# Optimization experiments

Hardware: AMD Instinct MI355X
Metric: run time of the kernel (lower is better)

The kernel has to match this reference:

```python
import jax, jax.numpy as jnp
import numpy as np

EPS = 1e-5        # torch LayerNorm default eps
INNER = 4
AFFECT_W = 0.3
BATCH = 65536
DIM = 128


def _ln(x, g, b):
    m = jnp.mean(x, axis=-1, keepdims=True)
    v = jnp.var(x, axis=-1, keepdims=True)
    return (x - m) * jax.lax.rsqrt(v + EPS) * g + b


def _gelu(x):
    return jax.nn.gelu(x, approximate=False)  # torch nn.GELU default (erf)


def setup_inputs() -> dict:
    key = jax.random.key(0)
    ks = jax.random.split(key, 18)
    B, d = BATCH, DIM

    def W(k, i, o):
        return jax.random.normal(k, (i, o), jnp.float32) / np.float32(np.sqrt(i))

    return {
        "x": jax.random.normal(ks[0], (B, d), jnp.float32),
        "y_init": jax.random.normal(ks[1], (B, d), jnp.float32),
        "affect_vec": jax.random.normal(ks[2], (B, 3), jnp.float32),
        "ln_latent_g": jnp.ones((3 * d,), jnp.float32), "ln_latent_b": jnp.zeros((3 * d,), jnp.float32),
        "ln_answer_g": jnp.ones((2 * d,), jnp.float32), "ln_answer_b": jnp.zeros((2 * d,), jnp.float32),
        "ln_z_g": jnp.ones((d,), jnp.float32), "ln_z_b": jnp.zeros((d,), jnp.float32),
        "lat_w1": W(ks[3], 3 * d, 2 * d), "lat_b1": jnp.zeros((2 * d,), jnp.float32),
        "lat_w2": W(ks[4], 2 * d, d), "lat_b2": jnp.zeros((d,), jnp.float32),
        "ans_w1": W(ks[5], 2 * d, 2 * d), "ans_b1": jnp.zeros((2 * d,), jnp.float32),
        "ans_w2": W(ks[6], 2 * d, d), "ans_b2": jnp.zeros((d,), jnp.float32),
        "aff_w": W(ks[7], 3, d), "aff_b": jnp.zeros((d,), jnp.float32),
        "gate_w": W(ks[8], 2 * d, 1), "gate_b": jnp.zeros((1,), jnp.float32),
        "q_w": W(ks[9], d, d), "q_b": jnp.zeros((d,), jnp.float32),
        "k_w": W(ks[10], d, d), "k_b": jnp.zeros((d,), jnp.float32),
        "v_w": W(ks[11], d, d), "v_b": jnp.zeros((d,), jnp.float32),
        "o_w": W(ks[12], d, d), "o_b": jnp.zeros((d,), jnp.float32),
        "pad_w1": W(ks[13], d, d // 2), "pad_b1": jnp.zeros((d // 2,), jnp.float32),
        "pad_w2": W(ks[14], d // 2, 3), "pad_b2": jnp.zeros((3,), jnp.float32),
        "K": 5,
    }


def _forward(x, y_init, affect_vec, ln_latent_g, ln_latent_b, ln_answer_g, ln_answer_b,
             ln_z_g, ln_z_b, lat_w1, lat_b1, lat_w2, lat_b2, ans_w1, ans_b1, ans_w2, ans_b2,
             aff_w, aff_b, gate_w, gate_b, q_w, q_b, k_w, k_b, v_w, v_b, o_w, o_b,
             pad_w1, pad_b1, pad_w2, pad_b2, K):
    d = x.shape[-1]
    scale = jnp.float32(d) ** -0.5
    y = y_init
    z = jnp.zeros_like(y)
    confs = []     # scalar gate means (detached, like .item() in torch)
    history = []   # list of [B, 1, d] z snapshots
    memory = []    # SoulKernel memory buffer: list of [d] rinse_state[0] snapshots
    for _ in range(K):
        for _ in range(INNER):
            li = _ln(jnp.concatenate([x, y, z], axis=-1), ln_latent_g, ln_latent_b)
            z_delta = _gelu(li @ lat_w1 + lat_b1) @ lat_w2 + lat_b2
            z = _ln(z + 0.3 * z_delta, ln_z_g, ln_z_b)
        affect_latent = jnp.tanh(affect_vec @ aff_w + aff_b)          # [B, d]
        gate = jax.nn.sigmoid(jnp.concatenate([z, affect_latent], axis=-1) @ gate_w + gate_b)  # [B, 1]
        z = z + AFFECT_W * gate * affect_latent
        confs.append(jax.lax.stop_gradient(jnp.mean(gate)))
        history.append(z[:, None, :])
        if len(history) > 1:
            seq = jnp.concatenate(history, axis=1)  # [B, t, d]
            Q = seq @ q_w + q_b
            Kt = seq @ k_w + k_b
            V = seq @ v_w + v_b
            attn = jax.nn.softmax(jnp.einsum('bsd,btd->bst', Q, Kt) * scale, axis=-1)
            attn_out = jnp.einsum('bst,btd->bsd', attn, V) @ o_w + o_b
            z = _ln(z + attn_out[:, -1, :], ln_z_g, ln_z_b)
        rinse = jnp.tanh(z + y)
        # SoulKernel (hope is computed but unused in the original)
        faith = jnp.sqrt(sum(confs) / len(confs))
        z = z + faith * 0.05 * z
        future = jnp.mean(jnp.stack(memory[-3:]), axis=0) if memory else jnp.zeros((d,), x.dtype)  # [d]
        bond = jnp.tanh(jax.lax.stop_gradient(jnp.mean(x * z)) + jax.lax.stop_gradient(jnp.mean(y * rinse)))
        z = z + 0.2 * bond * (future - z)
        rinse = jnp.tanh(rinse + future * 0.3)
        memory.append(jax.lax.stop_gradient(rinse[0]))
        ai = _ln(jnp.concatenate([y, z], axis=-1), ln_answer_g, ln_answer_b)
        y = y + 0.4 * (_gelu(ai @ ans_w1 + ans_b1) @ ans_w2 + ans_b2)
    pad = jnp.tanh(_gelu(z @ pad_w1 + pad_b1) @ pad_w2 + pad_b2)
    return y, jnp.stack(confs), pad


def reference(x, y_init, affect_vec, ln_latent_g, ln_latent_b, ln_answer_g, ln_answer_b,
              ln_z_g, ln_z_b, lat_w1, lat_b1, lat_w2, lat_b2, ans_w1, ans_b1, ans_w2, ans_b2,
              aff_w, aff_b, gate_w, gate_b, q_w, q_b, k_w, k_b, v_w, v_b, o_w, o_b,
              pad_w1, pad_b1, pad_w2, pad_b2, K):
    return _forward(x, y_init, affect_vec, ln_latent_g, ln_latent_b, ln_answer_g, ln_answer_b,
                    ln_z_g, ln_z_b, lat_w1, lat_b1, lat_w2, lat_b2, ans_w1, ans_b1, ans_w2, ans_b2,
                    aff_w, aff_b, gate_w, gate_b, q_w, q_b, k_w, k_b, v_w, v_b, o_w, o_b,
                    pad_w1, pad_b1, pad_w2, pad_b2, K)
```

## Files before the change

kernel.cpp:

```cpp
#include <hip/hip_runtime.h>
#include <math.h>


#define BATCH 65536
#define D 128
#define BD ((size_t)BATCH * D)
#define NSTEP 5
#define ROWS 32
#define NTHR 256
#define NBLK (BATCH / ROWS)
#define LN_EPS 1e-5f
#define ATT_SCALE 0.08838834764831845f
#define LDA 132
#define LDB 260

#define WS_Z    ((size_t)0)
#define WS_H1   (BD)
#define WS_PART (WS_H1 + 5*BD)
#define WS_SCAL (WS_PART + (size_t)NBLK*4)
#define WS_H2   (WS_SCAL + 2048)
#define WS_KV_END (WS_H2 + 5*BD)

#define SC_FS   0
#define SC_B02  1
#define SC_CSUM 2
#define SC_FUT  16
#define SC_MEM  256
#define SC_R10  960

struct Args {
  const float *x, *y_init, *affect;
  const float *g_lat, *b_lat, *g_ans, *b_ans, *g_z, *b_z;
  const float *lw1, *lb1, *lw2, *lb2;
  const float *aw1, *ab1, *aw2, *ab2;
  const float *affw, *affb, *gw, *gb;
  const float *qw, *qb, *kw, *kb, *vw, *vb, *ow, *ob;
  const float *pw1, *pb1, *pw2, *pb2;
  float *Y, *conf, *pad;
  float *Z, *H1, *H2, *PART, *SCAL;
  int useKV;
};

__device__ __forceinline__ float4 ld4(const float* p) { return *(const float4*)p; }
__device__ __forceinline__ void st4(float* p, float4 v) { *(float4*)p = v; }
__device__ __forceinline__ float geluf(float v) { return 0.5f*v*(1.0f + erff(v*0.70710678118654752f)); }
__device__ __forceinline__ float dot4(float4 a, float4 b){ return a.x*b.x + a.y*b.y + a.z*b.z + a.w*b.w; }
__device__ __forceinline__ void accSQ(float4 v, float& S, float& Q) {
  S += v.x+v.y+v.z+v.w;
  Q += v.x*v.x + v.y*v.y + v.z*v.z + v.w*v.w;
}

template<int KDIM, int NPT>
__device__ __forceinline__ void mm_block(const float* __restrict__ W, int N,
                                         const float* As, int lda,
                                         int rg, int cg, float (&acc)[4][NPT])
{
  const float* a0 = As + (rg*4+0)*lda;
  const float* a1 = As + (rg*4+1)*lda;
  const float* a2 = As + (rg*4+2)*lda;
  const float* a3 = As + (rg*4+3)*lda;
  const float* wp = W + cg*NPT;
  #pragma unroll 4
  for (int k = 0; k < KDIM; ++k) {
    float w[NPT];
    if constexpr (NPT == 8) {
      float4 w0 = ld4(wp + (size_t)k*N);
      float4 w1 = ld4(wp + (size_t)k*N + 4);
      w[0]=w0.x; w[1]=w0.y; w[2]=w0.z; w[3]=w0.w;
      w[4]=w1.x; w[5]=w1.y; w[6]=w1.z; w[7]=w1.w;
    } else if constexpr (NPT == 4) {
      float4 w0 = ld4(wp + (size_t)k*N);
      w[0]=w0.x; w[1]=w0.y; w[2]=w0.z; w[3]=w0.w;
    } else {
      float2 w0 = *(const float2*)(wp + (size_t)k*N);
      w[0]=w0.x; w[1]=w0.y;
    }
    float av0=a0[k], av1=a1[k], av2=a2[k], av3=a3[k];
    #pragma unroll
    for (int c = 0; c < NPT; ++c) {
      acc[0][c] += av0*w[c];
      acc[1][c] += av1*w[c];
      acc[2][c] += av2*w[c];
      acc[3][c] += av3*w[c];
    }
  }
}

__device__ __forceinline__ void z_ln_update(const Args& A, int row0, int rg, int cg,
                                            const float (&add)[4][4])
{
  float4 g4 = ld4(A.g_z + cg*4);
  float4 b4 = ld4(A.b_z + cg*4);
  #pragma unroll
  for (int rr = 0; rr < 4; ++rr) {
    size_t off = (size_t)(row0 + rg*4 + rr)*D + cg*4;
    float4 z = ld4(A.Z + off);
    float v0 = z.x + add[rr][0];
    float v1 = z.y + add[rr][1];
    float v2 = z.z + add[rr][2];
    float v3 = z.w + add[rr][3];
    float S = v0+v1+v2+v3;
    float Q = v0*v0+v1*v1+v2*v2+v3*v3;
    S += __shfl_xor(S,1);  Q += __shfl_xor(Q,1);
    S += __shfl_xor(S,2);  Q += __shfl_xor(Q,2);
    S += __shfl_xor(S,4);  Q += __shfl_xor(Q,4);
    S += __shfl_xor(S,8);  Q += __shfl_xor(Q,8);
    S += __shfl_xor(S,16); Q += __shfl_xor(Q,16);
    float m  = S*(1.f/128.f);
    float rs = rsqrtf(Q*(1.f/128.f) - m*m + LN_EPS);
    float4 o;
    o.x = (v0-m)*rs*g4.x + b4.x;
    o.y = (v1-m)*rs*g4.y + b4.y;
    o.z = (v2-m)*rs*g4.z + b4.z;
    o.w = (v3-m)*rs*g4.w + b4.w;
    st4(A.Z + off, o);
  }
}

__device__ __forceinline__ void stage_raw(float* sA, const float* src, int row0, int t)
{
  for (int e4 = t; e4 < ROWS*32; e4 += NTHR) {
    int r = e4 >> 5, c4 = e4 & 31;
    st4(sA + r*LDA + c4*4, ld4(src + (size_t)(row0+r)*D + c4*4));
  }
}

__device__ __forceinline__ void epilogue_phase(const Args& A, float* sB, float* sM, float* sR,
                                               int row0, int t, int rg, int cg, int r8, int sub)
{
  const float fs  = A.SCAL[SC_FS];
  const float b02 = A.SCAL[SC_B02];
  const float a   = fs*(1.0f - b02);
  for (int e4 = t; e4 < ROWS*32; e4 += NTHR) {
    int r = e4 >> 5, c4 = e4 & 31;
    size_t off = (size_t)(row0 + r)*D + c4*4;
    float4 z = ld4(A.Z + off);
    float4 f = ld4(A.SCAL + SC_FUT + c4*4);
    z.x = z.x*a + b02*f.x;
    z.y = z.y*a + b02*f.y;
    z.z = z.z*a + b02*f.z;
    z.w = z.w*a + b02*f.w;
    st4(A.Z + off, z);
  }
  __syncthreads();
  {
    const float* yr = A.Y + (size_t)(row0 + r8)*D;
    const float* zr = A.Z + (size_t)(row0 + r8)*D;
    float S = 0.f, Q = 0.f;
    #pragma unroll
    for (int j = 0; j < 4; ++j) {
      int c = (sub + 8*j)*4;
      accSQ(ld4(yr + c), S, Q);
      accSQ(ld4(zr + c), S, Q);
    }
    S += __shfl_xor(S,1); Q += __shfl_xor(Q,1);
    S += __shfl_xor(S,2); Q += __shfl_xor(Q,2);
    S += __shfl_xor(S,4); Q += __shfl_xor(Q,4);
    if (sub == 0) {
      float m = S*(1.f/256.f);
      sM[r8] = m;
      sR[r8] = rsqrtf(Q*(1.f/256.f) - m*m + LN_EPS);
    }
  }
  __syncthreads();
  for (int e4 = t; e4 < ROWS*64; e4 += NTHR) {
    int r = e4 >> 6, c4 = e4 & 63;
    int k = c4*4;
    float m = sM[r], rs = sR[r];
    float4 v = (k < D) ? ld4(A.Y + (size_t)(row0+r)*D + k)
                       : ld4(A.Z + (size_t)(row0+r)*D + (k - D));
    float4 g = ld4(A.g_ans + k);
    float4 b = ld4(A.b_ans + k);
    float4 o;
    o.x = (v.x-m)*rs*g.x + b.x;
    o.y = (v.y-m)*rs*g.y + b.y;
    o.z = (v.z-m)*rs*g.z + b.z;
    o.w = (v.w-m)*rs*g.w + b.w;
    st4(sB + r*LDB + k, o);
  }
  __syncthreads();
  float acc[4][8] = {};
  mm_block<256,8>(A.aw1, 256, sB, LDB, rg, cg, acc);
  float4 b1a = ld4(A.ab1 + cg*8);
  float4 b1b = ld4(A.ab1 + cg*8 + 4);
  float h[4][8];
  #pragma unroll
  for (int rr = 0; rr < 4; ++rr) {
    h[rr][0]=geluf(acc[rr][0]+b1a.x); h[rr][1]=geluf(acc[rr][1]+b1a.y);
    h[rr][2]=geluf(acc[rr][2]+b1a.z); h[rr][3]=geluf(acc[rr][3]+b1a.w);
    h[rr][4]=geluf(acc[rr][4]+b1b.x); h[rr][5]=geluf(acc[rr][5]+b1b.y);
    h[rr][6]=geluf(acc[rr][6]+b1b.z); h[rr][7]=geluf(acc[rr][7]+b1b.w);
  }
  __syncthreads();
  #pragma unroll
  for (int rr = 0; rr < 4; ++rr) {
    float4 h0; h0.x=h[rr][0]; h0.y=h[rr][1]; h0.z=h[rr][2]; h0.w=h[rr][3];
    float4 h1; h1.x=h[rr][4]; h1.y=h[rr][5]; h1.z=h[rr][6]; h1.w=h[rr][7];
    st4(sB + (rg*4+rr)*LDB + cg*8,     h0);
    st4(sB + (rg*4+rr)*LDB + cg*8 + 4, h1);
  }
  __syncthreads();
  float acc2[4][4] = {};
  mm_block<256,4>(A.aw2, 128, sB, LDB, rg, cg, acc2);
  float4 b2 = ld4(A.ab2 + cg*4);
  #pragma unroll
  for (int rr = 0; rr < 4; ++rr) {
    size_t off = (size_t)(row0 + rg*4 + rr)*D + cg*4;
    float4 y = ld4(A.Y + off);
    y.x += 0.4f*(acc2[rr][0] + b2.x);
    y.y += 0.4f*(acc2[rr][1] + b2.y);
    y.z += 0.4f*(acc2[rr][2] + b2.z);
    y.w += 0.4f*(acc2[rr][3] + b2.w);
    st4(A.Y + off, y);
  }
  __syncthreads();
}

__global__ void prepK(Args A)
{
  size_t i  = (size_t)blockIdx.x*blockDim.x + threadIdx.x;
  size_t n4 = BD/4;
  float4 zero; zero.x=0.f; zero.y=0.f; zero.z=0.f; zero.w=0.f;
  for (; i < n4; i += (size_t)gridDim.x*blockDim.x) {
    ((float4*)A.Z)[i] = zero;
    ((float4*)A.Y)[i] = ((const float4*)A.y_init)[i];
  }
}

template<int STEP>
__global__ __launch_bounds__(NTHR, 2) void stepK(Args A)
{
  __shared__ __align__(16) float sA[ROWS*LDA];
  __shared__ __align__(16) float sB[ROWS*LDB];
  __shared__ float sM[ROWS], sR[ROWS], sG[ROWS];
  __shared__ float sS[ROWS][8];
  __shared__ float sRed[4][2];

  const int t = threadIdx.x;
  const int row0 = blockIdx.x * ROWS;
  const int rg = t >> 5, cg = t & 31;
  const int r8 = t >> 3, sub = t & 7;

  if (STEP > 0)
    epilogue_phase(A, sB, sM, sR, row0, t, rg, cg, r8, sub);

  #pragma unroll 1
  for (int it = 0; it < 4; ++it) {
    {
      const float* xr = A.x + (size_t)(row0 + r8)*D;
      const float* yr = A.Y + (size_t)(row0 + r8)*D;
      const float* zr = A.Z + (size_t)(row0 + r8)*D;
      float S = 0.f, Q = 0.f;
      #pragma unroll
      for (int j = 0; j < 4; ++j) {
        int c = (sub + 8*j)*4;
        accSQ(ld4(xr + c), S, Q);
        accSQ(ld4(yr + c), S, Q);
        accSQ(ld4(zr + c), S, Q);
      }
      S += __shfl_xor(S,1); Q += __shfl_xor(Q,1);
      S += __shfl_xor(S,2); Q += __shfl_xor(Q,2);
      S += __shfl_xor(S,4); Q += __shfl_xor(Q,4);
      if (sub == 0) {
        float m = S*(1.f/384.f);
        sM[r8] = m;
        sR[r8] = rsqrtf(Q*(1.f/384.f) - m*m + LN_EPS);
      }
    }
    __syncthreads();
    float acc[4][8] = {};
    #pragma unroll 1
    for (int seg = 0; seg < 3; ++seg) {
      const float* src = (seg == 0) ? A.x : (seg == 1 ? (const float*)A.Y : (const float*)A.Z);
      for (int e4 = t; e4 < ROWS*32; e4 += NTHR) {
        int r = e4 >> 5, c4 = e4 & 31;
        float4 v = ld4(src + (size_t)(row0+r)*D + c4*4);
        float m = sM[r], rs = sR[r];
        int k = seg*D + c4*4;
        float4 g = ld4(A.g_lat + k);
        float4 b = ld4(A.b_lat + k);
        float4 o;
        o.x = (v.x-m)*rs*g.x + b.x;
        o.y = (v.y-m)*rs*g.y + b.y;
        o.z = (v.z-m)*rs*g.z + b.z;
        o.w = (v.w-m)*rs*g.w + b.w;
        st4(sA + r*LDA + c4*4, o);
      }
      __syncthreads();
      mm_block<128,8>(A.lw1 + (size_t)seg*D*256, 256, sA, LDA, rg, cg, acc);
      __syncthreads();
    }
    float4 l1a = ld4(A.lb1 + cg*8);
    float4 l1b = ld4(A.lb1 + cg*8 + 4);
    #pragma unroll
    for (int rr = 0; rr < 4; ++rr) {
      float4 h0, h1;
      h0.x = geluf(acc[rr][0]+l1a.x); h0.y = geluf(acc[rr][1]+l1a.y);
      h0.z = geluf(acc[rr][2]+l1a.z); h0.w = geluf(acc[rr][3]+l1a.w);
      h1.x = geluf(acc[rr][4]+l1b.x); h1.y = geluf(acc[rr][5]+l1b.y);
      h1.z = geluf(acc[rr][6]+l1b.z); h1.w = geluf(acc[rr][7]+l1b.w);
      st4(sB + (rg*4+rr)*LDB + cg*8,     h0);
      st4(sB + (rg*4+rr)*LDB + cg*8 + 4, h1);
    }
    __syncthreads();
    float acc2[4][4] = {};
    mm_block<256,4>(A.lw2, 128, sB, LDB, rg, cg, acc2);
    float4 l2 = ld4(A.lb2 + cg*4);
    float add[4][4];
    #pragma unroll
    for (int rr = 0; rr < 4; ++rr) {
      add[rr][0] = 0.3f*(acc2[rr][0]+l2.x);
      add[rr][1] = 0.3f*(acc2[rr][1]+l2.y);
      add[rr][2] = 0.3f*(acc2[rr][2]+l2.z);
      add[rr][3] = 0.3f*(acc2[rr][3]+l2.w);
    }
    z_ln_update(A, row0, rg, cg, add);
    __syncthreads();
  }

  {
    size_t row = (size_t)row0 + r8;
    const float* zr = A.Z + row*D;
    float af0 = A.affect[row*3+0];
    float af1 = A.affect[row*3+1];
    float af2 = A.affect[row*3+2];
    float dg = 0.f;
    #pragma unroll
    for (int j = 0; j < 4; ++j) {
      int c = (sub + 8*j)*4;
      float4 zv = ld4(zr + c);
      float4 g1 = ld4(A.gw + c);
      float4 g2 = ld4(A.gw + D + c);
      float4 w0 = ld4(A.affw + c);
      float4 w1 = ld4(A.affw + D + c);
      float4 w2 = ld4(A.affw + 2*D + c);
      float4 ab = ld4(A.affb + c);
      float4 al;
      al.x = tanhf(af0*w0.x + af1*w1.x + af2*w2.x + ab.x);
      al.y = tanhf(af0*w0.y + af1*w1.y + af2*w2.y + ab.y);
      al.z = tanhf(af0*w0.z + af1*w1.z + af2*w2.z + ab.z);
      al.w = tanhf(af0*w0.w + af1*w1.w + af2*w2.w + ab.w);
      st4(sA + r8*LDA + c, al);
      dg += dot4(zv, g1) + dot4(al, g2);
    }
    dg += __shfl_xor(dg,1);
    dg += __shfl_xor(dg,2);
    dg += __shfl_xor(dg,4);
    if (sub == 0) sG[r8] = 1.f/(1.f + expf(-(dg + A.gb[0])));
  }
  __syncthreads();
  {
    float* zhw = A.H1 + (size_t)STEP*BD;
    for (int e4 = t; e4 < ROWS*32; e4 += NTHR) {
      int r = e4 >> 5, c4 = e4 & 31;
      size_t off = (size_t)(row0+r)*D + c4*4;
      float4 z  = ld4(A.Z + off);
      float4 al = ld4(sA + r*LDA + c4*4);
      float g = 0.3f * sG[r];
      z.x += g*al.x; z.y += g*al.y; z.z += g*al.z; z.w += g*al.w;
      st4(A.Z + off, z);
      if (!A.useKV) st4(zhw + off, z);
    }
  }
  __syncthreads();

  float q[4][4];
  if (A.useKV || STEP > 0) {
    stage_raw(sA, A.Z, row0, t);
    __syncthreads();
  }
  if (A.useKV) {
    float kacc[4][4] = {}, vacc[4][4] = {};
    mm_block<128,4>(A.kw, 128, sA, LDA, rg, cg, kacc);
    mm_block<128,4>(A.vw, 128, sA, LDA, rg, cg, vacc);
    float4 kb4 = ld4(A.kb + cg*4);
    float4 vb4 = ld4(A.vb + cg*4);
    float* KH = A.H1 + (size_t)STEP*BD;
    float* VH = A.H2 + (size_t)STEP*BD;
    #pragma unroll
    for (int rr = 0; rr < 4; ++rr) {
      size_t off = (size_t)(row0 + rg*4 + rr)*D + cg*4;
      float4 kv; kv.x=kacc[rr][0]+kb4.x; kv.y=kacc[rr][1]+kb4.y;
                 kv.z=kacc[rr][2]+kb4.z; kv.w=kacc[rr][3]+kb4.w;
      float4 vv; vv.x=vacc[rr][0]+vb4.x; vv.y=vacc[rr][1]+vb4.y;
                 vv.z=vacc[rr][2]+vb4.z; vv.w=vacc[rr][3]+vb4.w;
      st4(KH + off, kv);
      st4(VH + off, vv);
    }
  }
  if (STEP > 0) {
    float qacc[4][4] = {};
    mm_block<128,4>(A.qw, 128, sA, LDA, rg, cg, qacc);
    float4 qb4 = ld4(A.qb + cg*4);
    #pragma unroll
    for (int rr = 0; rr < 4; ++rr) {
      q[rr][0]=qacc[rr][0]+qb4.x; q[rr][1]=qacc[rr][1]+qb4.y;
      q[rr][2]=qacc[rr][2]+qb4.z; q[rr][3]=qacc[rr][3]+qb4.w;
    }
  }

  if (STEP > 0) {
    if (A.useKV) {
      #pragma unroll 1
      for (int j = 0; j <= STEP; ++j) {
        const float* KH = A.H1 + (size_t)j*BD;
        #pragma unroll
        for (int rr = 0; rr < 4; ++rr) {
          float4 kv = ld4(KH + (size_t)(row0 + rg*4 + rr)*D + cg*4);
          float s = q[rr][0]*kv.x + q[rr][1]*kv.y + q[rr][2]*kv.z + q[rr][3]*kv.w;
          s += __shfl_xor(s,1); s += __shfl_xor(s,2); s += __shfl_xor(s,4);
          s += __shfl_xor(s,8); s += __shfl_xor(s,16);
          if (cg == 0) sS[rg*4+rr][j] = s;
        }
      }
    } else {
      #pragma unroll 1
      for (int j = 0; j <= STEP; ++j) {
        __syncthreads();
        stage_raw(sA, A.H1 + (size_t)j*BD, row0, t);
        __syncthreads();
        float kacc[4][4] = {};
        mm_block<128,4>(A.kw, 128, sA, LDA, rg, cg, kacc);
        float4 kb4 = ld4(A.kb + cg*4);
        #pragma unroll
        for (int rr = 0; rr < 4; ++rr) {
          float s = q[rr][0]*(kacc[rr][0]+kb4.x) + q[rr][1]*(kacc[rr][1]+kb4.y)
                  + q[rr][2]*(kacc[rr][2]+kb4.z) + q[rr][3]*(kacc[rr][3]+kb4.w);
          s += __shfl_xor(s,1); s += __shfl_xor(s,2); s += __shfl_xor(s,4);
          s += __shfl_xor(s,8); s += __shfl_xor(s,16);
          if (cg == 0) sS[rg*4+rr][j] = s;
        }
      }
    }
    __syncthreads();
    if (t < ROWS) {
      float mx = -3.0e38f;
      for (int j = 0; j <= STEP; ++j) { float v = sS[t][j]*ATT_SCALE; sS[t][j] = v; mx = fmaxf(mx, v); }
      float sum = 0.f;
      for (int j = 0; j <= STEP; ++j) { float p = expf(sS[t][j]-mx); sS[t][j] = p; sum += p; }
      float inv = 1.f/sum;
      for (int j = 0; j <= STEP; ++j) sS[t][j] *= inv;
    }
    __syncthreads();
    float ao[4][4] = {};
    if (A.useKV) {
      #pragma unroll 1
      for (int j = 0; j <= STEP; ++j) {
        const float* VH = A.H2 + (size_t)j*BD;
        #pragma unroll
        for (int rr = 0; rr < 4; ++rr) {
          float p = sS[rg*4+rr][j];
          float4 vv = ld4(VH + (size_t)(row0 + rg*4 + rr)*D + cg*4);
          ao[rr][0] += p*vv.x; ao[rr][1] += p*vv.y;
          ao[rr][2] += p*vv.z; ao[rr][3] += p*vv.w;
        }
      }
    } else {
      #pragma unroll 1
      for (int j = 0; j <= STEP; ++j) {
        __syncthreads();
        stage_raw(sA, A.H1 + (size_t)j*BD, row0, t);
        __syncthreads();
        float vacc[4][4] = {};
        mm_block<128,4>(A.vw, 128, sA, LDA, rg, cg, vacc);
        float4 vb4 = ld4(A.vb + cg*4);
        #pragma unroll
        for (int rr = 0; rr < 4; ++rr) {
          float p = sS[rg*4+rr][j];
          ao[rr][0] += p*(vacc[rr][0]+vb4.x);
          ao[rr][1] += p*(vacc[rr][1]+vb4.y);
          ao[rr][2] += p*(vacc[rr][2]+vb4.z);
          ao[rr][3] += p*(vacc[rr][3]+vb4.w);
        }
      }
      __syncthreads();
    }
    #pragma unroll
    for (int rr = 0; rr < 4; ++rr) {
      float4 v; v.x=ao[rr][0]; v.y=ao[rr][1]; v.z=ao[rr][2]; v.w=ao[rr][3];
      st4(sA + (rg*4+rr)*LDA + cg*4, v);
    }
    __syncthreads();
    float oacc[4][4] = {};
    mm_block<128,4>(A.ow, 128, sA, LDA, rg, cg, oacc);
    float4 ob4 = ld4(A.ob + cg*4);
    float add[4][4];
    #pragma unroll
    for (int rr = 0; rr < 4; ++rr) {
      add[rr][0] = oacc[rr][0]+ob4.x;
      add[rr][1] = oacc[rr][1]+ob4.y;
      add[rr][2] = oacc[rr][2]+ob4.z;
      add[rr][3] = oacc[rr][3]+ob4.w;
    }
    z_ln_update(A, row0, rg, cg, add);
    __syncthreads();
  }

  {
    float sxz = 0.f, syr = 0.f;
    for (int e4 = t; e4 < ROWS*32; e4 += NTHR) {
      int r = e4 >> 5, c4 = e4 & 31;
      size_t off = (size_t)(row0+r)*D + c4*4;
      float4 xv = ld4(A.x + off);
      float4 zv = ld4(A.Z + off);
      float4 yv = ld4(A.Y + off);
      float4 rn;
      rn.x = tanhf(zv.x + yv.x);
      rn.y = tanhf(zv.y + yv.y);
      rn.z = tanhf(zv.z + yv.z);
      rn.w = tanhf(zv.w + yv.w);
      sxz += dot4(xv, zv);
      syr += dot4(yv, rn);
      if (blockIdx.x == 0 && r == 0)
        st4(A.SCAL + SC_R10 + c4*4, rn);
    }
    #pragma unroll
    for (int m2 = 1; m2 < 64; m2 <<= 1) { sxz += __shfl_xor(sxz,m2); syr += __shfl_xor(syr,m2); }
    if ((t & 63) == 0) { sRed[t>>6][0] = sxz; sRed[t>>6][1] = syr; }
    __syncthreads();
    if (t == 0) {
      float X = 0.f, Yv = 0.f, G = 0.f;
      #pragma unroll
      for (int w2 = 0; w2 < 4; ++w2) { X += sRed[w2][0]; Yv += sRed[w2][1]; }
      #pragma unroll
      for (int r = 0; r < ROWS; ++r) G += sG[r];
      float* p = A.PART + (size_t)blockIdx.x*4;
      p[0] = G; p[1] = X; p[2] = Yv;
    }
  }
}

template<int STEP>
__global__ void redK(Args A)
{
  __shared__ float sRed[4][3];
  const int t = threadIdx.x;
  float sg = 0.f, sxz = 0.f, syr = 0.f;
  for (int b = t; b < NBLK; b += 256) {
    const float* p = A.PART + (size_t)b*4;
    sg += p[0]; sxz += p[1]; syr += p[2];
  }
  #pragma unroll
  for (int m = 1; m < 64; m <<= 1) {
    sg  += __shfl_xor(sg,m);
    sxz += __shfl_xor(sxz,m);
    syr += __shfl_xor(syr,m);
  }
  if ((t & 63) == 0) { int w = t>>6; sRed[w][0]=sg; sRed[w][1]=sxz; sRed[w][2]=syr; }
  __syncthreads();
  if (t == 0) {
    float G=0.f, X=0.f, Yv=0.f;
    #pragma unroll
    for (int w = 0; w < 4; ++w) { G += sRed[w][0]; X += sRed[w][1]; Yv += sRed[w][2]; }
    float conf = G * (1.f/(float)BATCH);
    float csum = conf + (STEP == 0 ? 0.f : A.SCAL[SC_CSUM]);
    A.SCAL[SC_CSUM] = csum;
    A.conf[STEP] = conf;
    float faith = sqrtf(csum / (float)(STEP+1));
    float fs = 1.f + 0.05f*faith;
    float bond = tanhf((fs*X + Yv) * (1.f/((float)BATCH*(float)D)));
    A.SCAL[SC_FS]  = fs;
    A.SCAL[SC_B02] = 0.2f*bond;
  }
  if (t < D) {
    float fut = 0.f;
    if (STEP > 0) {
      int lo = (STEP-3 < 0) ? 0 : STEP-3;
      float s = 0.f;
      for (int j = lo; j < STEP; ++j) s += A.SCAL[SC_MEM + j*D + t];
      fut = s / (float)(STEP - lo);
    }
    A.SCAL[SC_FUT + t] = fut;
    A.SCAL[SC_MEM + STEP*D + t] = tanhf(A.SCAL[SC_R10 + t] + 0.3f*fut);
  }
}

__global__ __launch_bounds__(NTHR, 2) void finalK(Args A)
{
  __shared__ __align__(16) float sA[ROWS*LDA];
  __shared__ __align__(16) float sB[ROWS*LDB];
  __shared__ float sM[ROWS], sR[ROWS];
  const int t = threadIdx.x;
  const int row0 = blockIdx.x * ROWS;
  const int rg = t >> 5, cg = t & 31;
  const int r8 = t >> 3, sub = t & 7;

  epilogue_phase(A, sB, sM, sR, row0, t, rg, cg, r8, sub);

  stage_raw(sA, A.Z, row0, t);
  __syncthreads();
  float acc[4][2] = {};
  mm_block<128,2>(A.pw1, 64, sA, LDA, rg, cg, acc);
  float2 pb = *(const float2*)(A.pb1 + cg*2);
  #pragma unroll
  for (int rr = 0; rr < 4; ++rr) {
    sB[(rg*4+rr)*LDB + cg*2 + 0] = geluf(acc[rr][0] + pb.x);
    sB[(rg*4+rr)*LDB + cg*2 + 1] = geluf(acc[rr][1] + pb.y);
  }
  __syncthreads();
  {
    float o0=0.f, o1=0.f, o2=0.f;
    #pragma unroll
    for (int jj = 0; jj < 8; ++jj) {
      int j = sub*8 + jj;
      float p = sB[r8*LDB + j];
      o0 += p*A.pw2[j*3+0];
      o1 += p*A.pw2[j*3+1];
      o2 += p*A.pw2[j*3+2];
    }
    o0 += __shfl_xor(o0,1); o0 += __shfl_xor(o0,2); o0 += __shfl_xor(o0,4);
    o1 += __shfl_xor(o1,1); o1 += __shfl_xor(o1,2); o1 += __shfl_xor(o1,4);
    o2 += __shfl_xor(o2,1); o2 += __shfl_xor(o2,2); o2 += __shfl_xor(o2,4);
    if (sub == 0) {
      size_t ro = (size_t)(row0 + r8)*3;
      A.pad[ro+0] = tanhf(o0 + A.pb2[0]);
      A.pad[ro+1] = tanhf(o1 + A.pb2[1]);
      A.pad[ro+2] = tanhf(o2 + A.pb2[2]);
    }
  }
}

extern "C" void kernel_launch(void* const* d_in, const int* in_sizes, int n_in,
                              void* d_out, int out_size, void* d_ws, size_t ws_size,
                              hipStream_t stream)
{
  (void)in_sizes; (void)n_in; (void)out_size;
  Args a;
  a.x      = (const float*)d_in[0];
  a.y_init = (const float*)d_in[1];
  a.affect = (const float*)d_in[2];
  a.g_lat  = (const float*)d_in[3];
  a.b_lat  = (const float*)d_in[4];
  a.g_ans  = (const float*)d_in[5];
  a.b_ans  = (const float*)d_in[6];
  a.g_z    = (const float*)d_in[7];
  a.b_z    = (const float*)d_in[8];
  a.lw1    = (const float*)d_in[9];
  a.lb1    = (const float*)d_in[10];
  a.lw2    = (const float*)d_in[11];
  a.lb2    = (const float*)d_in[12];
  a.aw1    = (const float*)d_in[13];
  a.ab1    = (const float*)d_in[14];
  a.aw2    = (const float*)d_in[15];
  a.ab2    = (const float*)d_in[16];
  a.affw   = (const float*)d_in[17];
  a.affb   = (const float*)d_in[18];
  a.gw     = (const float*)d_in[19];
  a.gb     = (const float*)d_in[20];
  a.qw     = (const float*)d_in[21];
  a.qb     = (const float*)d_in[22];
  a.kw     = (const float*)d_in[23];
  a.kb     = (const float*)d_in[24];
  a.vw     = (const float*)d_in[25];
  a.vb     = (const float*)d_in[26];
  a.ow     = (const float*)d_in[27];
  a.ob     = (const float*)d_in[28];
  a.pw1    = (const float*)d_in[29];
  a.pb1    = (const float*)d_in[30];
  a.pw2    = (const float*)d_in[31];
  a.pb2    = (const float*)d_in[32];
  float* out = (float*)d_out;
  a.Y    = out;
  a.conf = out + BD;
  a.pad  = a.conf + NSTEP;
  float* ws = (float*)d_ws;
  a.Z    = ws + WS_Z;
  a.H1   = ws + WS_H1;
  a.PART = ws + WS_PART;
  a.SCAL = ws + WS_SCAL;
  a.H2   = ws + WS_H2;
  a.useKV = (ws_size >= WS_KV_END * sizeof(float)) ? 1 : 0;

  prepK<<<dim3(2048), dim3(256), 0, stream>>>(a);
  stepK<0><<<dim3(NBLK), dim3(NTHR), 0, stream>>>(a);
  redK<0><<<dim3(1), dim3(256), 0, stream>>>(a);
  stepK<1><<<dim3(NBLK), dim3(NTHR), 0, stream>>>(a);
  redK<1><<<dim3(1), dim3(256), 0, stream>>>(a);
  stepK<2><<<dim3(NBLK), dim3(NTHR), 0, stream>>>(a);
  redK<2><<<dim3(1), dim3(256), 0, stream>>>(a);
  stepK<3><<<dim3(NBLK), dim3(NTHR), 0, stream>>>(a);
  redK<3><<<dim3(1), dim3(256), 0, stream>>>(a);
  stepK<4><<<dim3(NBLK), dim3(NTHR), 0, stream>>>(a);
  redK<4><<<dim3(1), dim3(256), 0, stream>>>(a);
  finalK<<<dim3(NBLK), dim3(NTHR), 0, stream>>>(a);
}
```

Baseline: 8.319 ms.

## Retile register GEMMs to 8 rows per thread with float4 LDS A loads

The shared-memory GEMM helper now reads four k-values of each A row with a single float4 LDS load and takes the row count per thread as a template parameter. The wide matmuls (256-output layers and the answer MLP) are remapped so each thread computes 8 rows by 4 or 2 columns instead of 4 rows by 8 or 4, which halves the per-thread global weight traffic. Launch bounds are raised from 2 to 3 blocks per SM to push occupancy higher. In exchange, LDS reads per thread rise and the tighter register budget risks spilling.

```diff
diff --git a/kernel.cpp b/kernel.cpp
--- a/kernel.cpp
+++ b/kernel.cpp
@@ -49,51 +49,57 @@
   S += v.x+v.y+v.z+v.w;
   Q += v.x*v.x + v.y*v.y + v.z*v.z + v.w*v.w;
 }
-
-template<int KDIM, int NPT>
+__device__ __forceinline__ float getf(const float4& v, int i) {
+  return i==0 ? v.x : (i==1 ? v.y : (i==2 ? v.z : v.w));
+}
+
+template<int KDIM, int NPT, int RPT>
 __device__ __forceinline__ void mm_block(const float* __restrict__ W, int N,
                                          const float* As, int lda,
-                                         int rg, int cg, float (&acc)[4][NPT])
-{
-  const float* a0 = As + (rg*4+0)*lda;
-  const float* a1 = As + (rg*4+1)*lda;
-  const float* a2 = As + (rg*4+2)*lda;
-  const float* a3 = As + (rg*4+3)*lda;
+                                         int rbase, int cg, float (&acc)[RPT][NPT])
+{
   const float* wp = W + cg*NPT;
-  #pragma unroll 4
-  for (int k = 0; k < KDIM; ++k) {
-    float w[NPT];
-    if constexpr (NPT == 8) {
-      float4 w0 = ld4(wp + (size_t)k*N);
-      float4 w1 = ld4(wp + (size_t)k*N + 4);
-      w[0]=w0.x; w[1]=w0.y; w[2]=w0.z; w[3]=w0.w;
-      w[4]=w1.x; w[5]=w1.y; w[6]=w1.z; w[7]=w1.w;
-    } else if constexpr (NPT == 4) {
-      float4 w0 = ld4(wp + (size_t)k*N);
-      w[0]=w0.x; w[1]=w0.y; w[2]=w0.z; w[3]=w0.w;
-    } else {
-      float2 w0 = *(const float2*)(wp + (size_t)k*N);
-      w[0]=w0.x; w[1]=w0.y;
-    }
-    float av0=a0[k], av1=a1[k], av2=a2[k], av3=a3[k];
-    #pragma unroll
-    for (int c = 0; c < NPT; ++c) {
-      acc[0][c] += av0*w[c];
-      acc[1][c] += av1*w[c];
-      acc[2][c] += av2*w[c];
-      acc[3][c] += av3*w[c];
-    }
-  }
-}
-
-__device__ __forceinline__ void z_ln_update(const Args& A, int row0, int rg, int cg,
+  #pragma unroll 2
+  for (int k4 = 0; k4 < KDIM/4; ++k4) {
+    float4 av[RPT];
+    #pragma unroll
+    for (int rr = 0; rr < RPT; ++rr)
+      av[rr] = ld4(As + (rbase+rr)*lda + k4*4);
+    #pragma unroll
+    for (int kk = 0; kk < 4; ++kk) {
+      const int k = k4*4 + kk;
+      float w[NPT];
+      if constexpr (NPT == 8) {
+        float4 w0 = ld4(wp + (size_t)k*N);
+        float4 w1 = ld4(wp + (size_t)k*N + 4);
+        w[0]=w0.x; w[1]=w0.y; w[2]=w0.z; w[3]=w0.w;
+        w[4]=w1.x; w[5]=w1.y; w[6]=w1.z; w[7]=w1.w;
+      } else if constexpr (NPT == 4) {
+        float4 w0 = ld4(wp + (size_t)k*N);
+        w[0]=w0.x; w[1]=w0.y; w[2]=w0.z; w[3]=w0.w;
+      } else {
+        float2 w0 = *(const float2*)(wp + (size_t)k*N);
+        w[0]=w0.x; w[1]=w0.y;
+      }
+      #pragma unroll
+      for (int rr = 0; rr < RPT; ++rr) {
+        float e = getf(av[rr], kk);
+        #pragma unroll
+        for (int c = 0; c < NPT; ++c)
+          acc[rr][c] += e*w[c];
+      }
+    }
+  }
+}
+
+__device__ __forceinline__ void z_ln_update(const Args& A, int row0, int rgO, int cgO,
                                             const float (&add)[4][4])
 {
-  float4 g4 = ld4(A.g_z + cg*4);
-  float4 b4 = ld4(A.b_z + cg*4);
+  float4 g4 = ld4(A.g_z + cgO*4);
+  float4 b4 = ld4(A.b_z + cgO*4);
   #pragma unroll
   for (int rr = 0; rr < 4; ++rr) {
-    size_t off = (size_t)(row0 + rg*4 + rr)*D + cg*4;
+    size_t off = (size_t)(row0 + rgO*4 + rr)*D + cgO*4;
     float4 z = ld4(A.Z + off);
     float v0 = z.x + add[rr][0];
     float v1 = z.y + add[rr][1];
@@ -126,7 +132,8 @@
 }
 
 __device__ __forceinline__ void epilogue_phase(const Args& A, float* sB, float* sM, float* sR,
-                                               int row0, int t, int rg, int cg, int r8, int sub)
+                                               int row0, int t, int rgN, int cgN,
+                                               int r8, int sub)
 {
   const float fs  = A.SCAL[SC_FS];
   const float b02 = A.SCAL[SC_B02];
@@ -179,39 +186,32 @@
     st4(sB + r*LDB + k, o);
   }
   __syncthreads();
-  float acc[4][8] = {};
-  mm_block<256,8>(A.aw1, 256, sB, LDB, rg, cg, acc);
-  float4 b1a = ld4(A.ab1 + cg*8);
-  float4 b1b = ld4(A.ab1 + cg*8 + 4);
-  float h[4][8];
+  float acc[8][4] = {};
+  mm_block<256,4,8>(A.aw1, 256, sB, LDB, rgN*8, cgN, acc);
+  float4 b1 = ld4(A.ab1 + cgN*4);
+  float h[8][4];
   #pragma unroll
-  for (int rr = 0; rr < 4; ++rr) {
-    h[rr][0]=geluf(acc[rr][0]+b1a.x); h[rr][1]=geluf(acc[rr][1]+b1a.y);
-    h[rr][2]=geluf(acc[rr][2]+b1a.z); h[rr][3]=geluf(acc[rr][3]+b1a.w);
-    h[rr][4]=geluf(acc[rr][4]+b1b.x); h[rr][5]=geluf(acc[rr][5]+b1b.y);
-    h[rr][6]=geluf(acc[rr][6]+b1b.z); h[rr][7]=geluf(acc[rr][7]+b1b.w);
+  for (int rr = 0; rr < 8; ++rr) {
+    h[rr][0]=geluf(acc[rr][0]+b1.x); h[rr][1]=geluf(acc[rr][1]+b1.y);
+    h[rr][2]=geluf(acc[rr][2]+b1.z); h[rr][3]=geluf(acc[rr][3]+b1.w);
   }
   __syncthreads();
   #pragma unroll
-  for (int rr = 0; rr < 4; ++rr) {
-    float4 h0; h0.x=h[rr][0]; h0.y=h[rr][1]; h0.z=h[rr][2]; h0.w=h[rr][3];
-    float4 h1; h1.x=h[rr][4]; h1.y=h[rr][5]; h1.z=h[rr][6]; h1.w=h[rr][7];
-    st4(sB + (rg*4+rr)*LDB + cg*8,     h0);
-    st4(sB + (rg*4+rr)*LDB + cg*8 + 4, h1);
-  }
-  __syncthreads();
-  float acc2[4][4] = {};
-  mm_block<256,4>(A.aw2, 128, sB, LDB, rg, cg, acc2);
-  float4 b2 = ld4(A.ab2 + cg*4);
+  for (int rr = 0; rr < 8; ++rr) {
+    float4 hv; hv.x=h[rr][0]; hv.y=h[rr][1]; hv.z=h[rr][2]; hv.w=h[rr][3];
+    st4(sB + (rgN*8+rr)*LDB + cgN*4, hv);
+  }
+  __syncthreads();
+  float acc2[8][2] = {};
+  mm_block<256,2,8>(A.aw2, 128, sB, LDB, rgN*8, cgN, acc2);
+  float2 b2 = *(const float2*)(A.ab2 + cgN*2);
   #pragma unroll
-  for (int rr = 0; rr < 4; ++rr) {
-    size_t off = (size_t)(row0 + rg*4 + rr)*D + cg*4;
-    float4 y = ld4(A.Y + off);
+  for (int rr = 0; rr < 8; ++rr) {
+    size_t off = (size_t)(row0 + rgN*8 + rr)*D + cgN*2;
+    float2 y = *(const float2*)(A.Y + off);
     y.x += 0.4f*(acc2[rr][0] + b2.x);
     y.y += 0.4f*(acc2[rr][1] + b2.y);
-    y.z += 0.4f*(acc2[rr][2] + b2.z);
-    y.w += 0.4f*(acc2[rr][3] + b2.w);
-    st4(A.Y + off, y);
+    *(float2*)(A.Y + off) = y;
   }
   __syncthreads();
 }
@@ -228,7 +228,7 @@
 }
 
 template<int STEP>
-__global__ __launch_bounds__(NTHR, 2) void stepK(Args A)
+__global__ __launch_bounds__(NTHR, 3) void stepK(Args A)
 {
   __shared__ __align__(16) float sA[ROWS*LDA];
   __shared__ __align__(16) float sB[ROWS*LDB];
@@ -238,11 +238,12 @@
 
   const int t = threadIdx.x;
   const int row0 = blockIdx.x * ROWS;
-  const int rg = t >> 5, cg = t & 31;
+  const int rgO = t >> 5, cgO = t & 31;
+  const int rgN = t >> 6, cgN = t & 63;
   const int r8 = t >> 3, sub = t & 7;
 
   if (STEP > 0)
-    epilogue_phase(A, sB, sM, sR, row0, t, rg, cg, r8, sub);
+    epilogue_phase(A, sB, sM, sR, row0, t, rgN, cgN, r8, sub);
 
   #pragma unroll 1
   for (int it = 0; it < 4; ++it) {
@@ -268,7 +269,7 @@
       }
     }
     __syncthreads();
-    float acc[4][8] = {};
+    float acc[8][4] = {};
     #pragma unroll 1
     for (int seg = 0; seg < 3; ++seg) {
       const float* src = (seg == 0) ? A.x : (seg == 1 ? (const float*)A.Y : (const float*)A.Z);
@@ -287,25 +288,23 @@
         st4(sA + r*LDA + c4*4, o);
       }
       __syncthreads();
-      mm_block<128,8>(A.lw1 + (size_t)seg*D*256, 256, sA, LDA, rg, cg, acc);
+      mm_block<128,4,8>(A.lw1 + (size_t)seg*D*256, 256, sA, LDA, rgN*8, cgN, acc);
       __syncthreads();
     }
-    float4 l1a = ld4(A.lb1 + cg*8);
-    float4 l1b = ld4(A.lb1 + cg*8 + 4);
-    #pragma unroll
-    for (int rr = 0; rr < 4; ++rr) {
-      float4 h0, h1;
-      h0.x = geluf(acc[rr][0]+l1a.x); h0.y = geluf(acc[rr][1]+l1a.y);
-      h0.z = geluf(acc[rr][2]+l1a.z); h0.w = geluf(acc[rr][3]+l1a.w);
-      h1.x = geluf(acc[rr][4]+l1b.x); h1.y = geluf(acc[rr][5]+l1b.y);
-      h1.z = geluf(acc[rr][6]+l1b.z); h1.w = geluf(acc[rr][7]+l1b.w);
-      st4(sB + (rg*4+rr)*LDB + cg*8,     h0);
-      st4(sB + (rg*4+rr)*LDB + cg*8 + 4, h1);
+    float4 l1 = ld4(A.lb1 + cgN*4);
+    #pragma unroll
+    for (int rr = 0; rr < 8; ++rr) {
+      float4 h;
+      h.x = geluf(acc[rr][0]+l1.x);
+      h.y = geluf(acc[rr][1]+l1.y);
+      h.z = geluf(acc[rr][2]+l1.z);
+      h.w = geluf(acc[rr][3]+l1.w);
+      st4(sB + (rgN*8+rr)*LDB + cgN*4, h);
     }
     __syncthreads();
     float acc2[4][4] = {};
-    mm_block<256,4>(A.lw2, 128, sB, LDB, rg, cg, acc2);
-    float4 l2 = ld4(A.lb2 + cg*4);
+    mm_block<256,4,4>(A.lw2, 128, sB, LDB, rgO*4, cgO, acc2);
+    float4 l2 = ld4(A.lb2 + cgO*4);
     float add[4][4];
     #pragma unroll
     for (int rr = 0; rr < 4; ++rr) {
@@ -314,7 +313,7 @@
       add[rr][2] = 0.3f*(acc2[rr][2]+l2.z);
       add[rr][3] = 0.3f*(acc2[rr][3]+l2.w);
     }
-    z_ln_update(A, row0, rg, cg, add);
+    z_ln_update(A, row0, rgO, cgO, add);
     __syncthreads();
   }
 
@@ -371,15 +370,15 @@
   }
   if (A.useKV) {
     float kacc[4][4] = {}, vacc[4][4] = {};
-    mm_block<128,4>(A.kw, 128, sA, LDA, rg, cg, kacc);
-    mm_block<128,4>(A.vw, 128, sA, LDA, rg, cg, vacc);
-    float4 kb4 = ld4(A.kb + cg*4);
-    float4 vb4 = ld4(A.vb + cg*4);
+    mm_block<128,4,4>(A.kw, 128, sA, LDA, rgO*4, cgO, kacc);
+    mm_block<128,4,4>(A.vw, 128, sA, LDA, rgO*4, cgO, vacc);
+    float4 kb4 = ld4(A.kb + cgO*4);
+    float4 vb4 = ld4(A.vb + cgO*4);
     float* KH = A.H1 + (size_t)STEP*BD;
     float* VH = A.H2 + (size_t)STEP*BD;
     #pragma unroll
     for (int rr = 0; rr < 4; ++rr) {
-      size_t off = (size_t)(row0 + rg*4 + rr)*D + cg*4;
+      size_t off = (size_t)(row0 + rgO*4 + rr)*D + cgO*4;
       float4 kv; kv.x=kacc[rr][0]+kb4.x; kv.y=kacc[rr][1]+kb4.y;
                  kv.z=kacc[rr][2]+kb4.z; kv.w=kacc[rr][3]+kb4.w;
       float4 vv; vv.x=vacc[rr][0]+vb4.x; vv.y=vacc[rr][1]+vb4.y;
@@ -390,8 +389,8 @@
   }
   if (STEP > 0) {
     float qacc[4][4] = {};
-    mm_block<128,4>(A.qw, 128, sA, LDA, rg, cg, qacc);
-    float4 qb4 = ld4(A.qb + cg*4);
+    mm_block<128,4,4>(A.qw, 128, sA, LDA, rgO*4, cgO, qacc);
+    float4 qb4 = ld4(A.qb + cgO*4);
     #pragma unroll
     for (int rr = 0; rr < 4; ++rr) {
       q[rr][0]=qacc[rr][0]+qb4.x; q[rr][1]=qacc[rr][1]+qb4.y;
@@ -406,11 +405,11 @@
         const float* KH = A.H1 + (size_t)j*BD;
         #pragma unroll
         for (int rr = 0; rr < 4; ++rr) {
-          float4 kv = ld4(KH + (size_t)(row0 + rg*4 + rr)*D + cg*4);
+          float4 kv = ld4(KH + (size_t)(row0 + rgO*4 + rr)*D + cgO*4);
           float s = q[rr][0]*kv.x + q[rr][1]*kv.y + q[rr][2]*kv.z + q[rr][3]*kv.w;
           s += __shfl_xor(s,1); s += __shfl_xor(s,2); s += __shfl_xor(s,4);
           s += __shfl_xor(s,8); s += __shfl_xor(s,16);
-          if (cg == 0) sS[rg*4+rr][j] = s;
+          if (cgO == 0) sS[rgO*4+rr][j] = s;
         }
       }
     } else {
@@ -420,15 +419,15 @@
         stage_raw(sA, A.H1 + (size_t)j*BD, row0, t);
         __syncthreads();
         float kacc[4][4] = {};
-        mm_block<128,4>(A.kw, 128, sA, LDA, rg, cg, kacc);
-        float4 kb4 = ld4(A.kb + cg*4);
+        mm_block<128,4,4>(A.kw, 128, sA, LDA, rgO*4, cgO, kacc);
+        float4 kb4 = ld4(A.kb + cgO*4);
         #pragma unroll
         for (int rr = 0; rr < 4; ++rr) {
           float s = q[rr][0]*(kacc[rr][0]+kb4.x) + q[rr][1]*(kacc[rr][1]+kb4.y)
                   + q[rr][2]*(kacc[rr][2]+kb4.z) + q[rr][3]*(kacc[rr][3]+kb4.w);
           s += __shfl_xor(s,1); s += __shfl_xor(s,2); s += __shfl_xor(s,4);
           s += __shfl_xor(s,8); s += __shfl_xor(s,16);
-          if (cg == 0) sS[rg*4+rr][j] = s;
+          if (cgO == 0) sS[rgO*4+rr][j] = s;
         }
       }
     }
@@ -449,8 +448,8 @@
         const float* VH = A.H2 + (size_t)j*BD;
         #pragma unroll
         for (int rr = 0; rr < 4; ++rr) {
-          float p = sS[rg*4+rr][j];
-          float4 vv = ld4(VH + (size_t)(row0 + rg*4 + rr)*D + cg*4);
+          float p = sS[rgO*4+rr][j];
+          float4 vv = ld4(VH + (size_t)(row0 + rgO*4 + rr)*D + cgO*4);
           ao[rr][0] += p*vv.x; ao[rr][1] += p*vv.y;
           ao[rr][2] += p*vv.z; ao[rr][3] += p*vv.w;
         }
@@ -462,11 +461,11 @@
         stage_raw(sA, A.H1 + (size_t)j*BD, row0, t);
         __syncthreads();
         float vacc[4][4] = {};
-        mm_block<128,4>(A.vw, 128, sA, LDA, rg, cg, vacc);
-        float4 vb4 = ld4(A.vb + cg*4);
+        mm_block<128,4,4>(A.vw, 128, sA, LDA, rgO*4, cgO, vacc);
+        float4 vb4 = ld4(A.vb + cgO*4);
         #pragma unroll
         for (int rr = 0; rr < 4; ++rr) {
-          float p = sS[rg*4+rr][j];
+          float p = sS[rgO*4+rr][j];
           ao[rr][0] += p*(vacc[rr][0]+vb4.x);
           ao[rr][1] += p*(vacc[rr][1]+vb4.y);
           ao[rr][2] += p*(vacc[rr][2]+vb4.z);
@@ -478,12 +477,12 @@
     #pragma unroll
     for (int rr = 0; rr < 4; ++rr) {
       float4 v; v.x=ao[rr][0]; v.y=ao[rr][1]; v.z=ao[rr][2]; v.w=ao[rr][3];
-      st4(sA + (rg*4+rr)*LDA + cg*4, v);
+      st4(sA + (rgO*4+rr)*LDA + cgO*4, v);
     }
     __syncthreads();
     float oacc[4][4] = {};
-    mm_block<128,4>(A.ow, 128, sA, LDA, rg, cg, oacc);
-    float4 ob4 = ld4(A.ob + cg*4);
+    mm_block<128,4,4>(A.ow, 128, sA, LDA, rgO*4, cgO, oacc);
+    float4 ob4 = ld4(A.ob + cgO*4);
     float add[4][4];
     #pragma unroll
     for (int rr = 0; rr < 4; ++rr) {
@@ -492,7 +491,7 @@
       add[rr][2] = oacc[rr][2]+ob4.z;
       add[rr][3] = oacc[rr][3]+ob4.w;
     }
-    z_ln_update(A, row0, rg, cg, add);
+    z_ln_update(A, row0, rgO, cgO, add);
     __syncthreads();
   }
 
@@ -575,27 +574,28 @@
   }
 }
 
-__global__ __launch_bounds__(NTHR, 2) void finalK(Args A)
+__global__ __launch_bounds__(NTHR, 3) void finalK(Args A)
 {
   __shared__ __align__(16) float sA[ROWS*LDA];
   __shared__ __align__(16) float sB[ROWS*LDB];
   __shared__ float sM[ROWS], sR[ROWS];
   const int t = threadIdx.x;
   const int row0 = blockIdx.x * ROWS;
-  const int rg = t >> 5, cg = t & 31;
+  const int rgO = t >> 5, cgO = t & 31;
+  const int rgN = t >> 6, cgN = t & 63;
   const int r8 = t >> 3, sub = t & 7;
 
-  epilogue_phase(A, sB, sM, sR, row0, t, rg, cg, r8, sub);
+  epilogue_phase(A, sB, sM, sR, row0, t, rgN, cgN, r8, sub);
 
   stage_raw(sA, A.Z, row0, t);
   __syncthreads();
   float acc[4][2] = {};
-  mm_block<128,2>(A.pw1, 64, sA, LDA, rg, cg, acc);
-  float2 pb = *(const float2*)(A.pb1 + cg*2);
+  mm_block<128,2,4>(A.pw1, 64, sA, LDA, rgO*4, cgO, acc);
+  float2 pb = *(const float2*)(A.pb1 + cgO*2);
   #pragma unroll
   for (int rr = 0; rr < 4; ++rr) {
-    sB[(rg*4+rr)*LDB + cg*2 + 0] = geluf(acc[rr][0] + pb.x);
-    sB[(rg*4+rr)*LDB + cg*2 + 1] = geluf(acc[rr][1] + pb.y);
+    sB[(rgO*4+rr)*LDB + cgO*2 + 0] = geluf(acc[rr][0] + pb.x);
+    sB[(rgO*4+rr)*LDB + cgO*2 + 1] = geluf(acc[rr][1] + pb.y);
   }
   __syncthreads();
   {
```

Result: faster. 7.309 ms (-12.1%).
